# Kernel tuning notes

Measured on AMD Instinct MI355X. Metric: run time of the kernel, lower is better.

## Reference

```python
import jax, jax.numpy as jnp
import numpy as np

NEG_INF = -1e30  # stand-in for float('-inf'); avoids inf-inf NaN edge cases, same softmax result


def setup_inputs() -> dict:
    key = jax.random.key(0)
    k1, k2, k3, k4, k5 = jax.random.split(key, 5)
    B, T, C, H = 16, 2048, 200, 64
    x = jax.random.normal(k1, (B, T, C), dtype=jnp.float32)
    # padding mask over key positions, broadcastable to [B, T, T]
    padding_mask = jax.random.randint(k2, (B, 1, T), 0, 2, dtype=jnp.int32)
    # nn.Linear(n_embd, head_size, bias=False) weights, stored as [C, H] so y = x @ W
    Wk = jax.random.normal(k3, (C, H), dtype=jnp.float32) * (C ** -0.5)
    Wq = jax.random.normal(k4, (C, H), dtype=jnp.float32) * (C ** -0.5)
    Wv = jax.random.normal(k5, (C, H), dtype=jnp.float32) * (C ** -0.5)
    return {"x": x, "padding_mask": padding_mask, "Wk": Wk, "Wq": Wq, "Wv": Wv}


def reference(x, padding_mask, Wk, Wq, Wv):
    # x: [B,T,C]; padding_mask: [B,1,T] (0 = padded key position)
    k = x @ Wk  # [B,T,H]
    q = x @ Wq  # [B,T,H]
    v = x @ Wv  # [B,T,H]
    scale = k.shape[-1] ** -0.5
    wei = jnp.einsum("bqh,bkh->bqk", q, k) * scale  # [B,T,T]
    # mask padded key columns before softmax
    wei = jnp.where(padding_mask == 0, NEG_INF, wei)
    wei = jax.nn.softmax(wei, axis=-1)
    # mask padded query rows (transpose of padding mask) to exact zero after softmax
    mask_t = jnp.swapaxes(padding_mask, -2, -1)  # [B,T,1]
    wei = jnp.where(mask_t == 0, 0.0, wei)
    # dropout is identity in eval mode
    out = jnp.einsum("bqk,bkh->bqh", wei, v)  # [B,T,H]
    return out
```

## Files before the change

kernel.cpp:

```cpp
#include <hip/hip_runtime.h>


typedef __attribute__((ext_vector_type(8))) __bf16 bf16x8;
typedef __attribute__((ext_vector_type(4))) __bf16 bf16x4;
typedef __attribute__((ext_vector_type(4))) float f32x4;

#define T_SEQ 2048
#define C_DIM 200
#define H_DIM 64
#define BT_TOT 32768
#define QKV_ELEMS 2097152
#define PPAD 72
#define OPAD 68
#define WTF_FULL 36864
#define WTF_ELEMS 38400
#define WTF_A_ELEMS 24576
#define LOG2E 1.44269504088896f

__global__ void prep_w(const float* __restrict__ Wk, const float* __restrict__ Wq,
                       const float* __restrict__ Wv, __bf16* __restrict__ WtF) {
    int idx = blockIdx.x * 256 + threadIdx.x;
    if (idx >= WTF_ELEMS) return;
    int w, c, h;
    if (idx < WTF_FULL) {
        int j = idx & 7, lane = (idx >> 3) & 63;
        int chunk = idx >> 9;
        int t = chunk & 3, rest = chunk >> 2;
        w = rest % 3; int ks = rest / 3;
        c = ks * 32 + (lane >> 4) * 8 + j;
        h = t * 16 + (lane & 15);
    } else {
        int i2 = idx - WTF_FULL;
        int j = i2 & 7, l15 = (i2 >> 3) & 15, t = (i2 >> 7) & 3;
        w = i2 >> 9;
        c = 192 + j;
        h = t * 16 + l15;
    }
    const float* W = (w == 0) ? Wq : (w == 1) ? Wk : Wv;
    float val = W[c * H_DIM + h];
    if (w == 0) val *= 0.125f * LOG2E;
    WtF[idx] = (__bf16)val;
}

__global__ __launch_bounds__(256) void qkv_proj(const float* __restrict__ x,
                                                const __bf16* __restrict__ WtF,
                                                __bf16* __restrict__ qb,
                                                __bf16* __restrict__ kb,
                                                __bf16* __restrict__ vT) {
    __shared__ __bf16 Wl[WTF_A_ELEMS];

    const int tid = threadIdx.x;
    const int wave = tid >> 6, lane = tid & 63, l15 = lane & 15, quad = lane >> 4;
    const int m0b = blockIdx.x * 64;
    const int row0 = m0b + wave * 16;

    f32x4 acc[3][4] = {};

    #pragma unroll
    for (int i = 0; i < 12; ++i) {
        const int c = i * 256 + tid;
        *(bf16x8*)(Wl + c * 8) = *(const bf16x8*)(WtF + c * 8);
    }
    __syncthreads();
    #pragma unroll
    for (int ks = 0; ks < 4; ++ks) {
        const float* xr = x + (size_t)(row0 + l15) * C_DIM + ks * 32 + quad * 8;
        const float4 f0 = *(const float4*)xr;
        const float4 f1 = *(const float4*)(xr + 4);
        bf16x8 a;
        a[0]=(__bf16)f0.x; a[1]=(__bf16)f0.y; a[2]=(__bf16)f0.z; a[3]=(__bf16)f0.w;
        a[4]=(__bf16)f1.x; a[5]=(__bf16)f1.y; a[6]=(__bf16)f1.z; a[7]=(__bf16)f1.w;
        #pragma unroll
        for (int w = 0; w < 3; ++w)
            #pragma unroll
            for (int t = 0; t < 4; ++t) {
                const bf16x8 bf = *(const bf16x8*)(Wl + ((ks * 12 + w * 4 + t) << 9) + lane * 8);
                acc[w][t] = __builtin_amdgcn_mfma_f32_16x16x32_bf16(a, bf, acc[w][t], 0, 0, 0);
            }
    }
    __syncthreads();

    #pragma unroll
    for (int i = 0; i < 7; ++i) {
        const int c = i * 256 + tid;
        if (c < 1728)
            *(bf16x8*)(Wl + c * 8) = *(const bf16x8*)(WtF + WTF_A_ELEMS + c * 8);
    }
    __syncthreads();
    #pragma unroll
    for (int ks = 4; ks < 7; ++ks) {
        bf16x8 a;
        if (ks < 6 || quad == 0) {
            const float* xr = x + (size_t)(row0 + l15) * C_DIM + ks * 32 + quad * 8;
            const float4 f0 = *(const float4*)xr;
            const float4 f1 = *(const float4*)(xr + 4);
            a[0]=(__bf16)f0.x; a[1]=(__bf16)f0.y; a[2]=(__bf16)f0.z; a[3]=(__bf16)f0.w;
            a[4]=(__bf16)f1.x; a[5]=(__bf16)f1.y; a[6]=(__bf16)f1.z; a[7]=(__bf16)f1.w;
        } else {
            #pragma unroll
            for (int j = 0; j < 8; ++j) a[j] = (__bf16)0.f;
        }
        #pragma unroll
        for (int w = 0; w < 3; ++w)
            #pragma unroll
            for (int t = 0; t < 4; ++t) {
                const int off = (ks < 6) ? (((ks - 4) * 12 + w * 4 + t) << 9) + lane * 8
                                         : 12288 + ((w * 4 + t) << 7) + l15 * 8;
                const bf16x8 bf = *(const bf16x8*)(Wl + off);
                acc[w][t] = __builtin_amdgcn_mfma_f32_16x16x32_bf16(a, bf, acc[w][t], 0, 0, 0);
            }
    }

    #pragma unroll
    for (int t = 0; t < 4; ++t)
        #pragma unroll
        for (int r = 0; r < 4; ++r) {
            const size_t m = row0 + quad * 4 + r;
            qb[m * H_DIM + t * 16 + l15] = (__bf16)acc[0][t][r];
            kb[m * H_DIM + t * 16 + l15] = (__bf16)acc[1][t][r];
        }
    __syncthreads();
    #pragma unroll
    for (int t = 0; t < 4; ++t)
        #pragma unroll
        for (int r = 0; r < 4; ++r)
            Wl[(t * 16 + l15) * 72 + wave * 16 + quad * 4 + r] = (__bf16)acc[2][t][r];
    __syncthreads();
    const int bb = m0b >> 11, tloc = m0b & 2047;
    #pragma unroll
    for (int i = 0; i < 2; ++i) {
        const int seg = i * 256 + tid;
        const int h = seg >> 3, s8 = seg & 7;
        *(bf16x8*)(vT + ((size_t)bb * H_DIM + h) * T_SEQ + tloc + s8 * 8) =
            *(const bf16x8*)(Wl + h * 72 + s8 * 8);
    }
}

__global__ __launch_bounds__(256, 2) void attn(const __bf16* __restrict__ qb,
                                               const __bf16* __restrict__ kb,
                                               const __bf16* __restrict__ vT,
                                               const int* __restrict__ pm,
                                               float* __restrict__ out) {
    __shared__ __align__(16) char arena[8192 + 36864];
    float* biasS = (float*)arena;

    const int tid = threadIdx.x;
    const int wave = tid >> 6, lane = tid & 63, l15 = lane & 15, quad = lane >> 4;
    const int ks = wave;
    const int b = blockIdx.y;
    const int q0 = blockIdx.x * 64;
    const size_t bT = (size_t)b * T_SEQ;

    for (int i = tid; i < 512; i += 256) {
        const int4 p4 = *(const int4*)(pm + bT + i * 4);
        biasS[i * 4 + 0] = p4.x ? 0.f : -1e30f;
        biasS[i * 4 + 1] = p4.y ? 0.f : -1e30f;
        biasS[i * 4 + 2] = p4.z ? 0.f : -1e30f;
        biasS[i * 4 + 3] = p4.w ? 0.f : -1e30f;
    }
    __syncthreads();

    bf16x8 qa[4][2];
    #pragma unroll
    for (int mt = 0; mt < 4; ++mt)
        #pragma unroll
        for (int s = 0; s < 2; ++s)
            qa[mt][s] = *(const bf16x8*)(qb + (bT + q0 + mt * 16 + l15) * H_DIM + s * 32 + quad * 8);

    __bf16* P = (__bf16*)(arena + 8192) + wave * (64 * PPAD);
    const __bf16* kbase = kb + bT * H_DIM;
    const __bf16* vbase = vT + (size_t)b * H_DIM * T_SEQ;

    f32x4 oacc[4][4] = {};
    float lsum[4] = {0.f, 0.f, 0.f, 0.f};

    bf16x8 kf[8];
    #pragma unroll
    for (int n = 0; n < 4; ++n)
        #pragma unroll
        for (int s = 0; s < 2; ++s)
            kf[n * 2 + s] = *(const bf16x8*)(kbase + (ks * 512 + n * 16 + l15) * H_DIM + s * 32 + quad * 8);

    for (int kt = 0; kt < 8; ++kt) {
        const int key0 = ks * 512 + kt * 64;

        bf16x8 vf[8];
        #pragma unroll
        for (int t = 0; t < 4; ++t)
            #pragma unroll
            for (int s = 0; s < 2; ++s)
                vf[t * 2 + s] = *(const bf16x8*)(vbase + (size_t)(t * 16 + l15) * T_SEQ + key0 + s * 32 + quad * 8);

        #pragma unroll
        for (int n = 0; n < 4; ++n) {
            const f32x4 bias = *(const f32x4*)(biasS + key0 + n * 16 + quad * 4);
            f32x4 s_[4];
            #pragma unroll
            for (int mt = 0; mt < 4; ++mt) s_[mt] = bias;
            #pragma unroll
            for (int s = 0; s < 2; ++s)
                #pragma unroll
                for (int mt = 0; mt < 4; ++mt)
                    s_[mt] = __builtin_amdgcn_mfma_f32_16x16x32_bf16(kf[n * 2 + s], qa[mt][s], s_[mt], 0, 0, 0);
            #pragma unroll
            for (int mt = 0; mt < 4; ++mt) {
                bf16x4 p4;
                #pragma unroll
                for (int r = 0; r < 4; ++r) {
                    const float e = exp2f(s_[mt][r]);
                    lsum[mt] += e;
                    p4[r] = (__bf16)e;
                }
                *(bf16x4*)(P + (mt * 16 + l15) * PPAD + n * 16 + quad * 4) = p4;
            }
        }

        const int keyn = ks * 512 + ((kt < 7) ? kt + 1 : 7) * 64;
        #pragma unroll
        for (int n = 0; n < 4; ++n)
            #pragma unroll
            for (int s = 0; s < 2; ++s)
                kf[n * 2 + s] = *(const bf16x8*)(kbase + (keyn + n * 16 + l15) * H_DIM + s * 32 + quad * 8);

        bf16x8 pa[4][2];
        #pragma unroll
        for (int mt = 0; mt < 4; ++mt)
            #pragma unroll
            for (int s = 0; s < 2; ++s)
                pa[mt][s] = *(const bf16x8*)(P + (mt * 16 + l15) * PPAD + s * 32 + quad * 8);

        #pragma unroll
        for (int t = 0; t < 4; ++t)
            #pragma unroll
            for (int s = 0; s < 2; ++s)
                #pragma unroll
                for (int mt = 0; mt < 4; ++mt)
                    oacc[mt][t] = __builtin_amdgcn_mfma_f32_16x16x32_bf16(pa[mt][s], vf[t * 2 + s], oacc[mt][t], 0, 0, 0);
    }

    #pragma unroll
    for (int mt = 0; mt < 4; ++mt) {
        lsum[mt] += __shfl_xor(lsum[mt], 16, 64);
        lsum[mt] += __shfl_xor(lsum[mt], 32, 64);
    }

    float* Ocomb = (float*)(arena + 8192);
    float* Lcomb = Ocomb + 64 * OPAD;

    __syncthreads();
    if (ks == 1) {
        #pragma unroll
        for (int mt = 0; mt < 4; ++mt) {
            #pragma unroll
            for (int t = 0; t < 4; ++t)
                #pragma unroll
                for (int r = 0; r < 4; ++r)
                    Ocomb[(mt * 16 + quad * 4 + r) * OPAD + t * 16 + l15] = oacc[mt][t][r];
            if (quad == 0) Lcomb[mt * 16 + l15] = lsum[mt];
        }
    }
    __syncthreads();
    if (ks == 2) {
        #pragma unroll
        for (int mt = 0; mt < 4; ++mt) {
            #pragma unroll
            for (int t = 0; t < 4; ++t)
                #pragma unroll
                for (int r = 0; r < 4; ++r)
                    Ocomb[(mt * 16 + quad * 4 + r) * OPAD + t * 16 + l15] += oacc[mt][t][r];
            if (quad == 0) Lcomb[mt * 16 + l15] += lsum[mt];
        }
    }
    __syncthreads();
    if (ks == 3) {
        #pragma unroll
        for (int mt = 0; mt < 4; ++mt) {
            #pragma unroll
            for (int t = 0; t < 4; ++t)
                #pragma unroll
                for (int r = 0; r < 4; ++r)
                    Ocomb[(mt * 16 + quad * 4 + r) * OPAD + t * 16 + l15] += oacc[mt][t][r];
            if (quad == 0) Lcomb[mt * 16 + l15] += lsum[mt];
        }
    }
    __syncthreads();
    if (ks == 0) {
        #pragma unroll
        for (int mt = 0; mt < 4; ++mt) {
            lsum[mt] += Lcomb[mt * 16 + l15];
            #pragma unroll
            for (int t = 0; t < 4; ++t)
                #pragma unroll
                for (int r = 0; r < 4; ++r)
                    oacc[mt][t][r] += Ocomb[(mt * 16 + quad * 4 + r) * OPAD + t * 16 + l15];
            #pragma unroll
            for (int r = 0; r < 4; ++r) {
                const int qpos = q0 + mt * 16 + quad * 4 + r;
                const float lv = __shfl(lsum[mt], quad * 4 + r, 64);
                const bool qvalid = biasS[qpos] == 0.f;
                const float inv = (qvalid && lv > 0.f) ? 1.f / lv : 0.f;
                #pragma unroll
                for (int t = 0; t < 4; ++t)
                    out[(bT + qpos) * H_DIM + t * 16 + l15] = oacc[mt][t][r] * inv;
            }
        }
    }
}

extern "C" void kernel_launch(void* const* d_in, const int* in_sizes, int n_in,
                              void* d_out, int out_size, void* d_ws, size_t ws_size,
                              hipStream_t stream) {
    const float* x  = (const float*)d_in[0];
    const int* pm   = (const int*)d_in[1];
    const float* Wk = (const float*)d_in[2];
    const float* Wq = (const float*)d_in[3];
    const float* Wv = (const float*)d_in[4];
    float* out = (float*)d_out;

    __bf16* qb  = (__bf16*)d_ws;
    __bf16* kb  = qb + QKV_ELEMS;
    __bf16* vT  = kb + QKV_ELEMS;
    __bf16* WtF = vT + QKV_ELEMS;

    prep_w<<<dim3((WTF_ELEMS + 255) / 256), dim3(256), 0, stream>>>(Wk, Wq, Wv, WtF);
    qkv_proj<<<dim3(BT_TOT / 64), dim3(256), 0, stream>>>(x, WtF, qb, kb, vT);
    attn<<<dim3(T_SEQ / 64, 16), dim3(256), 0, stream>>>(qb, kb, vT, pm, out);
}
```

Measured before the change: 124.5 us.

## Fuse weight prep into QKV projection and double attention query tile

Removes the separate prep_w kernel: each qkv_proj block now reads fp32 weights directly, scales Wq, and scatters them as bf16 into the LDS fragment layout. The attention kernel processes 128 queries per block instead of 64, so each K/V fragment load is reused across twice as many query tiles. The K/V register prefetch is dropped and replaced by loads inside the inner loops. The cross-wave reduction now finalises output with all four waves, each writing two row tiles from shared memory. In exchange the attention kernel uses much more LDS and registers (launch bounds lowered to 1), halves the grid to 256 blocks, and every projection block redundantly converts the weights with uncoalesced LDS scatter writes.

Result: slower. 142.8 us (+14.7%).

```diff
diff --git a/kernel.cpp b/kernel.cpp
--- a/kernel.cpp
+++ b/kernel.cpp
@@ -12,42 +12,16 @@
 #define QKV_ELEMS 2097152
 #define PPAD 72
 #define OPAD 68
-#define WTF_FULL 36864
-#define WTF_ELEMS 38400
-#define WTF_A_ELEMS 24576
 #define LOG2E 1.44269504088896f
 
-__global__ void prep_w(const float* __restrict__ Wk, const float* __restrict__ Wq,
-                       const float* __restrict__ Wv, __bf16* __restrict__ WtF) {
-    int idx = blockIdx.x * 256 + threadIdx.x;
-    if (idx >= WTF_ELEMS) return;
-    int w, c, h;
-    if (idx < WTF_FULL) {
-        int j = idx & 7, lane = (idx >> 3) & 63;
-        int chunk = idx >> 9;
-        int t = chunk & 3, rest = chunk >> 2;
-        w = rest % 3; int ks = rest / 3;
-        c = ks * 32 + (lane >> 4) * 8 + j;
-        h = t * 16 + (lane & 15);
-    } else {
-        int i2 = idx - WTF_FULL;
-        int j = i2 & 7, l15 = (i2 >> 3) & 15, t = (i2 >> 7) & 3;
-        w = i2 >> 9;
-        c = 192 + j;
-        h = t * 16 + l15;
-    }
-    const float* W = (w == 0) ? Wq : (w == 1) ? Wk : Wv;
-    float val = W[c * H_DIM + h];
-    if (w == 0) val *= 0.125f * LOG2E;
-    WtF[idx] = (__bf16)val;
-}
-
-__global__ __launch_bounds__(256) void qkv_proj(const float* __restrict__ x,
-                                                const __bf16* __restrict__ WtF,
+__global__ __launch_bounds__(256) void qkv_proj(const float* __restrict__ Wk,
+                                                const float* __restrict__ Wq,
+                                                const float* __restrict__ Wv,
+                                                const float* __restrict__ x,
                                                 __bf16* __restrict__ qb,
                                                 __bf16* __restrict__ kb,
                                                 __bf16* __restrict__ vT) {
-    __shared__ __bf16 Wl[WTF_A_ELEMS];
+    __shared__ __bf16 Wl[24576];
 
     const int tid = threadIdx.x;
     const int wave = tid >> 6, lane = tid & 63, l15 = lane & 15, quad = lane >> 4;
@@ -57,9 +31,16 @@
     f32x4 acc[3][4] = {};
 
     #pragma unroll
-    for (int i = 0; i < 12; ++i) {
-        const int c = i * 256 + tid;
-        *(bf16x8*)(Wl + c * 8) = *(const bf16x8*)(WtF + c * 8);
+    for (int w = 0; w < 3; ++w) {
+        const float* W = (w == 0) ? Wq : (w == 1) ? Wk : Wv;
+        const float scale = (w == 0) ? 0.125f * LOG2E : 1.f;
+        for (int i = tid; i < 8192; i += 256) {
+            const int c = i >> 6, h = i & 63;
+            const float val = W[i] * scale;
+            const int ks = c >> 5, cq = (c >> 3) & 3, j = c & 7;
+            const int t = h >> 4, hl = h & 15;
+            Wl[((ks * 12 + w * 4 + t) << 9) + (cq * 16 + hl) * 8 + j] = (__bf16)val;
+        }
     }
     __syncthreads();
     #pragma unroll
@@ -81,10 +62,22 @@
     __syncthreads();
 
     #pragma unroll
-    for (int i = 0; i < 7; ++i) {
-        const int c = i * 256 + tid;
-        if (c < 1728)
-            *(bf16x8*)(Wl + c * 8) = *(const bf16x8*)(WtF + WTF_A_ELEMS + c * 8);
+    for (int w = 0; w < 3; ++w) {
+        const float* W = (w == 0) ? Wq : (w == 1) ? Wk : Wv;
+        const float scale = (w == 0) ? 0.125f * LOG2E : 1.f;
+        for (int i = tid; i < 4608; i += 256) {
+            const int c = 128 + (i >> 6), h = i & 63;
+            const float val = W[c * H_DIM + h] * scale;
+            const int t = h >> 4, hl = h & 15;
+            int addr;
+            if (c < 192) {
+                const int ks = c >> 5, cq = (c >> 3) & 3, j = c & 7;
+                addr = (((ks - 4) * 12 + w * 4 + t) << 9) + (cq * 16 + hl) * 8 + j;
+            } else {
+                addr = 12288 + ((w * 4 + t) << 7) + hl * 8 + (c - 192);
+            }
+            Wl[addr] = (__bf16)val;
+        }
     }
     __syncthreads();
     #pragma unroll
@@ -136,19 +129,19 @@
     }
 }
 
-__global__ __launch_bounds__(256, 2) void attn(const __bf16* __restrict__ qb,
+__global__ __launch_bounds__(256, 1) void attn(const __bf16* __restrict__ qb,
                                                const __bf16* __restrict__ kb,
                                                const __bf16* __restrict__ vT,
                                                const int* __restrict__ pm,
                                                float* __restrict__ out) {
-    __shared__ __align__(16) char arena[8192 + 36864];
+    __shared__ __align__(16) char arena[8192 + 73728];
     float* biasS = (float*)arena;
 
     const int tid = threadIdx.x;
     const int wave = tid >> 6, lane = tid & 63, l15 = lane & 15, quad = lane >> 4;
     const int ks = wave;
     const int b = blockIdx.y;
-    const int q0 = blockIdx.x * 64;
+    const int q0 = blockIdx.x * 128;
     const size_t bT = (size_t)b * T_SEQ;
 
     for (int i = tid; i < 512; i += 256) {
@@ -160,50 +153,40 @@
     }
     __syncthreads();
 
-    bf16x8 qa[4][2];
-    #pragma unroll
-    for (int mt = 0; mt < 4; ++mt)
+    bf16x8 qa[8][2];
+    #pragma unroll
+    for (int mt = 0; mt < 8; ++mt)
         #pragma unroll
         for (int s = 0; s < 2; ++s)
             qa[mt][s] = *(const bf16x8*)(qb + (bT + q0 + mt * 16 + l15) * H_DIM + s * 32 + quad * 8);
 
-    __bf16* P = (__bf16*)(arena + 8192) + wave * (64 * PPAD);
+    __bf16* P = (__bf16*)(arena + 8192) + wave * (128 * PPAD);
     const __bf16* kbase = kb + bT * H_DIM;
     const __bf16* vbase = vT + (size_t)b * H_DIM * T_SEQ;
 
-    f32x4 oacc[4][4] = {};
-    float lsum[4] = {0.f, 0.f, 0.f, 0.f};
-
-    bf16x8 kf[8];
-    #pragma unroll
-    for (int n = 0; n < 4; ++n)
-        #pragma unroll
-        for (int s = 0; s < 2; ++s)
-            kf[n * 2 + s] = *(const bf16x8*)(kbase + (ks * 512 + n * 16 + l15) * H_DIM + s * 32 + quad * 8);
+    f32x4 oacc[8][4] = {};
+    float lsum[8] = {};
 
     for (int kt = 0; kt < 8; ++kt) {
         const int key0 = ks * 512 + kt * 64;
 
-        bf16x8 vf[8];
-        #pragma unroll
-        for (int t = 0; t < 4; ++t)
-            #pragma unroll
-            for (int s = 0; s < 2; ++s)
-                vf[t * 2 + s] = *(const bf16x8*)(vbase + (size_t)(t * 16 + l15) * T_SEQ + key0 + s * 32 + quad * 8);
-
         #pragma unroll
         for (int n = 0; n < 4; ++n) {
             const f32x4 bias = *(const f32x4*)(biasS + key0 + n * 16 + quad * 4);
-            f32x4 s_[4];
-            #pragma unroll
-            for (int mt = 0; mt < 4; ++mt) s_[mt] = bias;
+            bf16x8 kf[2];
+            #pragma unroll
+            for (int s = 0; s < 2; ++s)
+                kf[s] = *(const bf16x8*)(kbase + (key0 + n * 16 + l15) * H_DIM + s * 32 + quad * 8);
+            f32x4 s_[8];
+            #pragma unroll
+            for (int mt = 0; mt < 8; ++mt) s_[mt] = bias;
             #pragma unroll
             for (int s = 0; s < 2; ++s)
                 #pragma unroll
-                for (int mt = 0; mt < 4; ++mt)
-                    s_[mt] = __builtin_amdgcn_mfma_f32_16x16x32_bf16(kf[n * 2 + s], qa[mt][s], s_[mt], 0, 0, 0);
-            #pragma unroll
-            for (int mt = 0; mt < 4; ++mt) {
+                for (int mt = 0; mt < 8; ++mt)
+                    s_[mt] = __builtin_amdgcn_mfma_f32_16x16x32_bf16(kf[s], qa[mt][s], s_[mt], 0, 0, 0);
+            #pragma unroll
+            for (int mt = 0; mt < 8; ++mt) {
                 bf16x4 p4;
                 #pragma unroll
                 for (int r = 0; r < 4; ++r) {
@@ -215,94 +198,76 @@
             }
         }
 
-        const int keyn = ks * 512 + ((kt < 7) ? kt + 1 : 7) * 64;
-        #pragma unroll
-        for (int n = 0; n < 4; ++n)
-            #pragma unroll
-            for (int s = 0; s < 2; ++s)
-                kf[n * 2 + s] = *(const bf16x8*)(kbase + (keyn + n * 16 + l15) * H_DIM + s * 32 + quad * 8);
-
-        bf16x8 pa[4][2];
-        #pragma unroll
-        for (int mt = 0; mt < 4; ++mt)
+        bf16x8 pa[8][2];
+        #pragma unroll
+        for (int mt = 0; mt < 8; ++mt)
             #pragma unroll
             for (int s = 0; s < 2; ++s)
                 pa[mt][s] = *(const bf16x8*)(P + (mt * 16 + l15) * PPAD + s * 32 + quad * 8);
 
         #pragma unroll
-        for (int t = 0; t < 4; ++t)
+        for (int t = 0; t < 4; ++t) {
+            bf16x8 vf[2];
+            #pragma unroll
+            for (int s = 0; s < 2; ++s)
+                vf[s] = *(const bf16x8*)(vbase + (size_t)(t * 16 + l15) * T_SEQ + key0 + s * 32 + quad * 8);
             #pragma unroll
             for (int s = 0; s < 2; ++s)
                 #pragma unroll
-                for (int mt = 0; mt < 4; ++mt)
-                    oacc[mt][t] = __builtin_amdgcn_mfma_f32_16x16x32_bf16(pa[mt][s], vf[t * 2 + s], oacc[mt][t], 0, 0, 0);
-    }
-
-    #pragma unroll
-    for (int mt = 0; mt < 4; ++mt) {
+                for (int mt = 0; mt < 8; ++mt)
+                    oacc[mt][t] = __builtin_amdgcn_mfma_f32_16x16x32_bf16(pa[mt][s], vf[s], oacc[mt][t], 0, 0, 0);
+        }
+    }
+
+    #pragma unroll
+    for (int mt = 0; mt < 8; ++mt) {
         lsum[mt] += __shfl_xor(lsum[mt], 16, 64);
         lsum[mt] += __shfl_xor(lsum[mt], 32, 64);
     }
 
     float* Ocomb = (float*)(arena + 8192);
-    float* Lcomb = Ocomb + 64 * OPAD;
-
-    __syncthreads();
-    if (ks == 1) {
-        #pragma unroll
-        for (int mt = 0; mt < 4; ++mt) {
+    float* Lcomb = Ocomb + 128 * OPAD;
+
+    __syncthreads();
+    #pragma unroll
+    for (int step = 0; step < 4; ++step) {
+        const int who = (step == 3) ? 0 : step + 1;
+        if (ks == who) {
+            #pragma unroll
+            for (int mt = 0; mt < 8; ++mt) {
+                if (step == 0) {
+                    #pragma unroll
+                    for (int t = 0; t < 4; ++t)
+                        #pragma unroll
+                        for (int r = 0; r < 4; ++r)
+                            Ocomb[(mt * 16 + quad * 4 + r) * OPAD + t * 16 + l15] = oacc[mt][t][r];
+                    if (quad == 0) Lcomb[mt * 16 + l15] = lsum[mt];
+                } else {
+                    #pragma unroll
+                    for (int t = 0; t < 4; ++t)
+                        #pragma unroll
+                        for (int r = 0; r < 4; ++r)
+                            Ocomb[(mt * 16 + quad * 4 + r) * OPAD + t * 16 + l15] += oacc[mt][t][r];
+                    if (quad == 0) Lcomb[mt * 16 + l15] += lsum[mt];
+                }
+            }
+        }
+        __syncthreads();
+    }
+
+    #pragma unroll
+    for (int mi = 0; mi < 2; ++mi) {
+        const int mt = ks * 2 + mi;
+        #pragma unroll
+        for (int r = 0; r < 4; ++r) {
+            const int qpos = q0 + mt * 16 + quad * 4 + r;
+            const float lv = Lcomb[mt * 16 + quad * 4 + r];
+            const bool qvalid = biasS[qpos] == 0.f;
+            const float inv = (qvalid && lv > 0.f) ? 1.f / lv : 0.f;
             #pragma unroll
             for (int t = 0; t < 4; ++t)
-                #pragma unroll
-                for (int r = 0; r < 4; ++r)
-                    Ocomb[(mt * 16 + quad * 4 + r) * OPAD + t * 16 + l15] = oacc[mt][t][r];
-            if (quad == 0) Lcomb[mt * 16 + l15] = lsum[mt];
-        }
-    }
-    __syncthreads();
-    if (ks == 2) {
-        #pragma unroll
-        for (int mt = 0; mt < 4; ++mt) {
-            #pragma unroll
-            for (int t = 0; t < 4; ++t)
-                #pragma unroll
-                for (int r = 0; r < 4; ++r)
-                    Ocomb[(mt * 16 + quad * 4 + r) * OPAD + t * 16 + l15] += oacc[mt][t][r];
-            if (quad == 0) Lcomb[mt * 16 + l15] += lsum[mt];
-        }
-    }
-    __syncthreads();
-    if (ks == 3) {
-        #pragma unroll
-        for (int mt = 0; mt < 4; ++mt) {
-            #pragma unroll
-            for (int t = 0; t < 4; ++t)
-                #pragma unroll
-                for (int r = 0; r < 4; ++r)
-                    Ocomb[(mt * 16 + quad * 4 + r) * OPAD + t * 16 + l15] += oacc[mt][t][r];
-            if (quad == 0) Lcomb[mt * 16 + l15] += lsum[mt];
-        }
-    }
-    __syncthreads();
-    if (ks == 0) {
-        #pragma unroll
-        for (int mt = 0; mt < 4; ++mt) {
-            lsum[mt] += Lcomb[mt * 16 + l15];
-            #pragma unroll
-            for (int t = 0; t < 4; ++t)
-                #pragma unroll
-                for (int r = 0; r < 4; ++r)
-                    oacc[mt][t][r] += Ocomb[(mt * 16 + quad * 4 + r) * OPAD + t * 16 + l15];
-            #pragma unroll
-            for (int r = 0; r < 4; ++r) {
-                const int qpos = q0 + mt * 16 + quad * 4 + r;
-                const float lv = __shfl(lsum[mt], quad * 4 + r, 64);
-                const bool qvalid = biasS[qpos] == 0.f;
-                const float inv = (qvalid && lv > 0.f) ? 1.f / lv : 0.f;
-                #pragma unroll
-                for (int t = 0; t < 4; ++t)
-                    out[(bT + qpos) * H_DIM + t * 16 + l15] = oacc[mt][t][r] * inv;
-            }
+                out[(bT + qpos) * H_DIM + t * 16 + l15] =
+                    Ocomb[(mt * 16 + quad * 4 + r) * OPAD + t * 16 + l15] * inv;
         }
     }
 }
@@ -317,12 +282,10 @@
     const float* Wv = (const float*)d_in[4];
     float* out = (float*)d_out;
 
-    __bf16* qb  = (__bf16*)d_ws;
-    __bf16* kb  = qb + QKV_ELEMS;
-    __bf16* vT  = kb + QKV_ELEMS;
-    __bf16* WtF = vT + QKV_ELEMS;
-
-    prep_w<<<dim3((WTF_ELEMS + 255) / 256), dim3(256), 0, stream>>>(Wk, Wq, Wv, WtF);
-    qkv_proj<<<dim3(BT_TOT / 64), dim3(256), 0, stream>>>(x, WtF, qb, kb, vT);
-    attn<<<dim3(T_SEQ / 64, 16), dim3(256), 0, stream>>>(qb, kb, vT, pm, out);
+    __bf16* qb = (__bf16*)d_ws;
+    __bf16* kb = qb + QKV_ELEMS;
+    __bf16* vT = kb + QKV_ELEMS;
+
+    qkv_proj<<<dim3(BT_TOT / 64), dim3(256), 0, stream>>>(Wk, Wq, Wv, x, qb, kb, vT);
+    attn<<<dim3(T_SEQ / 128, 16), dim3(256), 0, stream>>>(qb, kb, vT, pm, out);
 }
```
